# Optimization experiments

Hardware: AMD Instinct MI355X
Metric: run time of the kernel (lower is better)

Reference implementation:

```python
import jax, jax.numpy as jnp
import numpy as np

N = 50000      # nodes
E = 800000     # edges (before self loops)
F_IN = 128     # dataset.num_features
HID = 32       # hidden_channels (per GAT head)
HEADS = 4
C = 40         # dataset.num_classes
NEG_SLOPE = 0.2


def setup_inputs() -> dict:
    key = jax.random.key(0)
    ks = jax.random.split(key, 18)
    g = lambda k, shape, fan: jax.random.normal(k, shape, dtype=jnp.float32) / np.sqrt(fan)
    inp = {
        "x": jax.random.normal(ks[0], (N, F_IN), dtype=jnp.float32),
        "edge_index": jax.random.randint(ks[1], (2, E), 0, N, dtype=jnp.int64),
        # GAT layer 1: F_IN -> HEADS*HID
        "gat_W1": g(ks[2], (F_IN, HEADS * HID), F_IN),
        "gat_att_src1": g(ks[3], (HEADS, HID), HID),
        "gat_att_dst1": g(ks[4], (HEADS, HID), HID),
        "gat_b1": jnp.zeros((HEADS * HID,), jnp.float32),
        # GAT layer 2: HEADS*HID -> C, heads=1
        "gat_W2": g(ks[5], (HEADS * HID, C), HEADS * HID),
        "gat_att_src2": g(ks[6], (1, C), C),
        "gat_att_dst2": g(ks[7], (1, C), C),
        "gat_b2": jnp.zeros((C,), jnp.float32),
        # GCN layers
        "gcn_W1": g(ks[8], (F_IN, HID), F_IN),
        "gcn_b1": jnp.zeros((HID,), jnp.float32),
        "gcn_W2": g(ks[9], (HID, C), HID),
        "gcn_b2": jnp.zeros((C,), jnp.float32),
        # final linear: 2C -> C
        "lin_W": g(ks[10], (2 * C, C), 2 * C),
        "lin_b": jnp.zeros((C,), jnp.float32),
        "weight_c": jnp.float32(0.5),
        "weight_t": jnp.float32(0.5),
    }
    return inp


def _add_self_loops(src, dst, n):
    loop = jnp.arange(n, dtype=src.dtype)
    return jnp.concatenate([src, loop]), jnp.concatenate([dst, loop])


def _gat_conv(x, src, dst, n, W, att_src, att_dst, b, heads, out_dim):
    # h: [n, heads, out_dim]
    h = (x @ W).reshape(n, heads, out_dim)
    a_s = jnp.einsum('nhd,hd->nh', h, att_src)   # source-side attention logit
    a_d = jnp.einsum('nhd,hd->nh', h, att_dst)   # target-side attention logit
    e = jax.nn.leaky_relu(a_s[src] + a_d[dst], NEG_SLOPE)  # [E', heads]
    # softmax over incoming edges of each target node (self loops guarantee >=1 edge)
    m = jax.ops.segment_max(e, dst, num_segments=n)
    ex = jnp.exp(e - m[dst])
    s = jax.ops.segment_sum(ex, dst, num_segments=n)
    alpha = ex / s[dst]                          # [E', heads]
    out = jax.ops.segment_sum(h[src] * alpha[..., None], dst, num_segments=n)
    return out.reshape(n, heads * out_dim) + b


def _gcn_conv(x, src, dst, n, W, b):
    h = x @ W
    deg = jax.ops.segment_sum(jnp.ones(src.shape, h.dtype), dst, num_segments=n)
    norm = jax.lax.rsqrt(deg)                    # deg >= 1 (self loops)
    coef = (norm[src] * norm[dst])[:, None]
    return jax.ops.segment_sum(h[src] * coef, dst, num_segments=n) + b


def reference(x, edge_index, gat_W1, gat_att_src1, gat_att_dst1, gat_b1,
              gat_W2, gat_att_src2, gat_att_dst2, gat_b2,
              gcn_W1, gcn_b1, gcn_W2, gcn_b2, lin_W, lin_b,
              weight_c, weight_t):
    n = x.shape[0]
    src, dst = _add_self_loops(edge_index[0], edge_index[1], n)
    # GAT branch (dropout is identity at inference)
    x_gat = _gat_conv(x, src, dst, n, gat_W1, gat_att_src1, gat_att_dst1,
                      gat_b1, HEADS, HID)
    x_gat = jax.nn.elu(x_gat)
    x_gat = _gat_conv(x_gat, src, dst, n, gat_W2, gat_att_src2, gat_att_dst2,
                      gat_b2, 1, C)
    # GCN branch
    x_gcn = jax.nn.relu(_gcn_conv(x, src, dst, n, gcn_W1, gcn_b1))
    x_gcn = _gcn_conv(x_gcn, src, dst, n, gcn_W2, gcn_b2)
    # weighted feature concat + linear head
    cat = jnp.concatenate([x_gcn * weight_c, x_gat * weight_t], axis=1)  # [n, 2C]
    return cat @ lin_W + lin_b
```

## Files before the change

kernel.cpp:

```cpp
#include <hip/hip_runtime.h>
#include <math.h>

#define F_IN   128
#define HIDC   32
#define NHEAD  4
#define CDIM   40
#define NEG_SLOPE 0.2f
#define BCAP   4096
#define OVCAP  16384
#define SCHUNK 4096

typedef __attribute__((ext_vector_type(8))) short bf16x8;
typedef __attribute__((ext_vector_type(4))) float f32x4;

__device__ __forceinline__ float leakyf(float x) { return x > 0.f ? x : NEG_SLOPE * x; }

__device__ __forceinline__ float wred_sum(float v) {
#pragma unroll
    for (int o = 32; o > 0; o >>= 1) v += __shfl_xor(v, o, 64);
    return v;
}
__device__ __forceinline__ float sel4(float4 v, int h) {
    return (h == 0) ? v.x : (h == 1) ? v.y : (h == 2) ? v.z : v.w;
}
__device__ __forceinline__ unsigned pack2_bf16(float a, float b) {
    unsigned ua = __float_as_uint(a);
    unsigned ub = __float_as_uint(b);
    ua = (ua + 0x7FFFu + ((ua >> 16) & 1u)) >> 16;
    ub = (ub + 0x7FFFu + ((ub >> 16) & 1u)) >> 16;
    return ua | (ub << 16);
}
__device__ __forceinline__ float2 unpack2_bf16(unsigned p) {
    return make_float2(__uint_as_float(p << 16), __uint_as_float(p & 0xFFFF0000u));
}
__device__ __forceinline__ float bf2f(unsigned short u) {
    return __uint_as_float(((unsigned)u) << 16);
}

__global__ void wb_prep_kernel(const float* __restrict__ Wg, const float* __restrict__ Wc,
                               uint4* __restrict__ wbf)
{
    int b = blockIdx.x;
    int lane = threadIdx.x;
    int nt = b >> 2, ks = b & 3;
    int c = nt * 16 + (lane & 15);
    int k0 = ks * 32 + (lane >> 4) * 8;
    unsigned u[4];
#pragma unroll
    for (int jj = 0; jj < 4; ++jj) {
        int k = k0 + 2 * jj;
        float a0 = (c < 128) ? Wg[(size_t)k * 128 + c] : Wc[(size_t)k * 32 + (c - 128)];
        float a1 = (c < 128) ? Wg[(size_t)(k + 1) * 128 + c] : Wc[(size_t)(k + 1) * 32 + (c - 128)];
        u[jj] = pack2_bf16(a0, a1);
    }
    wbf[(size_t)b * 64 + lane] = make_uint4(u[0], u[1], u[2], u[3]);
}

__global__ __launch_bounds__(256) void gemm1_mfma_kernel(
    const float* __restrict__ X, const uint4* __restrict__ wbf,
    const float* __restrict__ aw_s, const float* __restrict__ aw_d,
    unsigned* __restrict__ h1g,
    float* __restrict__ as1, float* __restrict__ ad1, int n)
{
    __shared__ float Ct[64][164];
    __shared__ float sw[128], dw[128];
    const int tid = threadIdx.x;
    const int w = tid >> 6, lane = tid & 63;
    const int m = lane & 15, q = lane >> 4;
    const int node0 = blockIdx.x * 64;
    if (tid < 128) { sw[tid] = aw_s[tid]; dw[tid] = aw_d[tid]; }

    f32x4 acc[10];
#pragma unroll
    for (int t = 0; t < 10; ++t) acc[t] = (f32x4){0.f, 0.f, 0.f, 0.f};

    const int row = node0 + w * 16 + m;
    const bool rv = row < n;
#pragma unroll
    for (int ks = 0; ks < 4; ++ks) {
        uint4 pa = make_uint4(0u, 0u, 0u, 0u);
        if (rv) {
            const float* xr = X + (size_t)row * 128 + ks * 32 + q * 8;
            float4 a0 = *(const float4*)xr;
            float4 a1 = *(const float4*)(xr + 4);
            pa = make_uint4(pack2_bf16(a0.x, a0.y), pack2_bf16(a0.z, a0.w),
                            pack2_bf16(a1.x, a1.y), pack2_bf16(a1.z, a1.w));
        }
        bf16x8 af = *(bf16x8*)&pa;
#pragma unroll
        for (int nt = 0; nt < 10; ++nt) {
            uint4 pb = wbf[(size_t)(nt * 4 + ks) * 64 + lane];
            bf16x8 bfv = *(bf16x8*)&pb;
            acc[nt] = __builtin_amdgcn_mfma_f32_16x16x32_bf16(af, bfv, acc[nt], 0, 0, 0);
        }
    }
#pragma unroll
    for (int nt = 0; nt < 10; ++nt)
#pragma unroll
        for (int r = 0; r < 4; ++r)
            Ct[w * 16 + q * 4 + r][nt * 16 + m] = acc[nt][r];
    __syncthreads();

    for (int i = tid; i < 64 * 80; i += 256) {
        int nd = i / 80, u = i - nd * 80;
        int gn = node0 + nd;
        if (gn < n)
            h1g[(size_t)gn * 80 + u] = pack2_bf16(Ct[nd][2 * u], Ct[nd][2 * u + 1]);
    }
    {
        int nd = tid >> 2, h = tid & 3;
        int gn = node0 + nd;
        if (gn < n) {
            float s = 0.f, d = 0.f;
#pragma unroll
            for (int k = 0; k < HIDC; ++k) {
                float v = Ct[nd][h * HIDC + k];
                s = fmaf(v, sw[h * HIDC + k], s);
                d = fmaf(v, dw[h * HIDC + k], d);
            }
            as1[(size_t)gn * 4 + h] = s;
            ad1[(size_t)gn * 4 + h] = d;
        }
    }
}

__global__ __launch_bounds__(256) void bucket_scatter_kernel(
    const int* __restrict__ src, const int* __restrict__ dst,
    unsigned* __restrict__ bcnt, unsigned* __restrict__ bpair,
    unsigned* __restrict__ ovf_cnt, uint2* __restrict__ ovf, int e, int nbuck)
{
    __shared__ unsigned hist[512];
    __shared__ unsigned base[512];
    const int t = threadIdx.x;
    const int lo = blockIdx.x * SCHUNK;
    const int hi = min(lo + SCHUNK, e);
    for (int i = t; i < nbuck; i += 256) hist[i] = 0;
    __syncthreads();
    for (int i = lo + t; i < hi; i += 256)
        atomicAdd(&hist[((unsigned)dst[i]) >> 7], 1u);
    __syncthreads();
    for (int i = t; i < nbuck; i += 256) {
        unsigned c = hist[i];
        base[i] = c ? atomicAdd(&bcnt[i], c) : 0u;
        hist[i] = 0;
    }
    __syncthreads();
    for (int i = lo + t; i < hi; i += 256) {
        unsigned s = (unsigned)src[i], d = (unsigned)dst[i];
        unsigned b = d >> 7;
        unsigned pos = base[b] + atomicAdd(&hist[b], 1u);
        if (pos < BCAP) bpair[(size_t)b * BCAP + pos] = s | ((d & 127u) << 16);
        else {
            unsigned o = atomicAdd(ovf_cnt, 1u);
            if (o < OVCAP) ovf[o] = make_uint2(s, d);
        }
    }
}

__global__ __launch_bounds__(256) void bucket_count_kernel(
    const unsigned* __restrict__ bcnt, const unsigned* __restrict__ bpair,
    const unsigned* __restrict__ ovf_cnt, const uint2* __restrict__ ovf,
    unsigned* __restrict__ counts, int n)
{
    __shared__ unsigned lc[128];
    const int b = blockIdx.x, base = b << 7;
    if (threadIdx.x < 128) lc[threadIdx.x] = 0;
    __syncthreads();
    unsigned bc = bcnt[b];
    int cnt = (int)(bc < BCAP ? bc : BCAP);
    for (int k = threadIdx.x; k < cnt; k += 256)
        atomicAdd(&lc[bpair[(size_t)b * BCAP + k] >> 16], 1u);
    unsigned oc_u = *ovf_cnt;
    int oc = (int)(oc_u < OVCAP ? oc_u : OVCAP);
    for (int k = threadIdx.x; k < oc; k += 256) {
        uint2 pp = ovf[k];
        if ((int)(pp.y >> 7) == b) atomicAdd(&lc[pp.y & 127u], 1u);
    }
    __syncthreads();
    int i = base + threadIdx.x;
    if (threadIdx.x < 128 && i < n) counts[i] = lc[threadIdx.x];
}

__global__ __launch_bounds__(256) void scan_reduce_kernel(const unsigned* __restrict__ counts,
                                                          unsigned* __restrict__ partials, int n)
{
    __shared__ unsigned sm[256];
    int t = threadIdx.x;
    int i = blockIdx.x * 256 + t;
    unsigned v = (i < n) ? counts[i] : 0u;
    sm[t] = v;
    __syncthreads();
#pragma unroll
    for (int off = 128; off > 0; off >>= 1) {
        if (t < off) sm[t] += sm[t + off];
        __syncthreads();
    }
    if (t == 0) partials[blockIdx.x] = sm[0];
}

__global__ __launch_bounds__(256) void scan_partials_kernel(unsigned* __restrict__ partials,
                                                            unsigned* __restrict__ rs, int nb, int n)
{
    __shared__ unsigned sm[256];
    int t = threadIdx.x;
    unsigned v = (t < nb) ? partials[t] : 0u;
    sm[t] = v;
    __syncthreads();
#pragma unroll
    for (int off = 1; off < 256; off <<= 1) {
        unsigned u = (t >= off) ? sm[t - off] : 0u;
        __syncthreads();
        sm[t] += u;
        __syncthreads();
    }
    if (t < nb) partials[t] = sm[t] - v;
    if (t == 255) rs[n] = sm[255];
}

__global__ __launch_bounds__(256) void scan_write_kernel(const unsigned* __restrict__ counts,
                                                         const unsigned* __restrict__ partials,
                                                         unsigned* __restrict__ rs,
                                                         float* __restrict__ nrm, int n)
{
    __shared__ unsigned sm[256];
    int t = threadIdx.x;
    int i = blockIdx.x * 256 + t;
    unsigned c = (i < n) ? counts[i] : 0u;
    sm[t] = c;
    __syncthreads();
#pragma unroll
    for (int off = 1; off < 256; off <<= 1) {
        unsigned u = (t >= off) ? sm[t - off] : 0u;
        __syncthreads();
        sm[t] += u;
        __syncthreads();
    }
    if (i < n) {
        rs[i] = partials[blockIdx.x] + sm[t] - c;
        nrm[i] = rsqrtf((float)(c + 1u));
    }
}

__global__ __launch_bounds__(256) void bucket_place_kernel(
    const unsigned* __restrict__ bcnt, const unsigned* __restrict__ bpair,
    const unsigned* __restrict__ rs, unsigned* __restrict__ csr_src,
    unsigned* __restrict__ cursor, int n)
{
    __shared__ unsigned lc[128];
    __shared__ unsigned rbase[128];
    const int b = blockIdx.x, base = b << 7;
    if (threadIdx.x < 128) {
        lc[threadIdx.x] = 0;
        int i = base + threadIdx.x;
        rbase[threadIdx.x] = (i < n) ? rs[i] : 0u;
    }
    __syncthreads();
    unsigned bc = bcnt[b];
    int cnt = (int)(bc < BCAP ? bc : BCAP);
    for (int k = threadIdx.x; k < cnt; k += 256) {
        unsigned v = bpair[(size_t)b * BCAP + k];
        unsigned ld = v >> 16;
        unsigned r = atomicAdd(&lc[ld], 1u);
        csr_src[rbase[ld] + r] = v & 0xFFFFu;
    }
    __syncthreads();
    int i = base + threadIdx.x;
    if (threadIdx.x < 128 && i < n) cursor[i] = rbase[threadIdx.x] + lc[threadIdx.x];
}

__global__ void overflow_fill_kernel(const unsigned* __restrict__ ovf_cnt,
                                     const uint2* __restrict__ ovf,
                                     unsigned* __restrict__ cursor,
                                     unsigned* __restrict__ csr_src)
{
    unsigned oc_u = *ovf_cnt;
    int oc = (int)(oc_u < OVCAP ? oc_u : OVCAP);
    for (int k = threadIdx.x; k < oc; k += 256) {
        uint2 pp = ovf[k];
        unsigned pos = atomicAdd(&cursor[pp.y], 1u);
        csr_src[pos] = pp.x;
    }
}

#define CAP1 96
__global__ __launch_bounds__(256) void agg1_fused_kernel(
    const unsigned* __restrict__ h1g,
    const float* __restrict__ as1, const float* __restrict__ ad1,
    const float* __restrict__ nrm,
    const unsigned* __restrict__ rs, const unsigned* __restrict__ csr_src,
    const float* __restrict__ gat_b1, const float* __restrict__ gcn_b1,
    unsigned* __restrict__ xgb, unsigned* __restrict__ gaccb, int n)
{
    __shared__ uint2 scA[4][CAP1];
    __shared__ float w4[4][CAP1][4];
    const int wid = threadIdx.x >> 6;
    const int lane = threadIdx.x & 63;
    const int i = blockIdx.x * 4 + wid;
    if (i >= n) return;
    const unsigned beg = rs[i];
    const int deg = (int)(rs[i + 1] - beg);
    const float4* as1v = (const float4*)as1;
    float4 av = as1v[i];
    float4 dv = ((const float4*)ad1)[i];
    const float ni = nrm[i];
    float4 ese = make_float4(__expf(leakyf(av.x + dv.x)), __expf(leakyf(av.y + dv.y)),
                             __expf(leakyf(av.z + dv.z)), __expf(leakyf(av.w + dv.w)));
    float s0 = 0.f, s1 = 0.f, s2 = 0.f, s3 = 0.f;
    for (int k = lane; k < deg; k += 64) {
        unsigned s = csr_src[beg + k];
        float4 a = as1v[s];
        float w0 = __expf(leakyf(a.x + dv.x)), w1 = __expf(leakyf(a.y + dv.y));
        float w2 = __expf(leakyf(a.z + dv.z)), w3 = __expf(leakyf(a.w + dv.w));
        if (k < CAP1) {
            scA[wid][k] = make_uint2(s, __float_as_uint(nrm[s]));
            w4[wid][k][0] = w0; w4[wid][k][1] = w1;
            w4[wid][k][2] = w2; w4[wid][k][3] = w3;
        }
        s0 += w0; s1 += w1; s2 += w2; s3 += w3;
    }
    if (lane == 0) { s0 += ese.x; s1 += ese.y; s2 += ese.z; s3 += ese.w; }
    s0 = wred_sum(s0); s1 = wred_sum(s1); s2 = wred_sum(s2); s3 = wred_sum(s3);
    __threadfence_block();
    const int h = lane >> 4;
    const float advh = sel4(dv, h);
    const float ssh  = sel4(make_float4(s0, s1, s2, s3), h);
    const float wself = sel4(ese, h);
    const bool gact = lane < 32;
    const unsigned short* h1s = (const unsigned short*)h1g;
    float2 hv = unpack2_bf16(h1g[(size_t)i * 80 + lane]);
    float2 acc = make_float2(hv.x * wself, hv.y * wself);
    float gacc = gact ? bf2f(h1s[(size_t)i * 160 + 128 + lane]) * ni * ni : 0.f;
    const int dcB = deg < CAP1 ? deg : CAP1;
    int j = 0;
    for (; j + 4 <= dcB; j += 4) {
        uint2 sc[4]; float ww[4];
#pragma unroll
        for (int t = 0; t < 4; ++t) {
            sc[t] = scA[wid][j + t];
            ww[t] = w4[wid][j + t][h];
        }
        unsigned pv[4];
#pragma unroll
        for (int t = 0; t < 4; ++t) pv[t] = h1g[(size_t)sc[t].x * 80 + lane];
        float gv[4];
        if (gact) {
#pragma unroll
            for (int t = 0; t < 4; ++t) gv[t] = bf2f(h1s[(size_t)sc[t].x * 160 + 128 + lane]);
        }
#pragma unroll
        for (int t = 0; t < 4; ++t) {
            float2 v = unpack2_bf16(pv[t]);
            acc.x = fmaf(v.x, ww[t], acc.x);
            acc.y = fmaf(v.y, ww[t], acc.y);
            if (gact) gacc = fmaf(gv[t], __uint_as_float(sc[t].y) * ni, gacc);
        }
    }
    for (; j < dcB; ++j) {
        uint2 sc = scA[wid][j];
        float w = w4[wid][j][h];
        float2 v = unpack2_bf16(h1g[(size_t)sc.x * 80 + lane]);
        acc.x = fmaf(v.x, w, acc.x);
        acc.y = fmaf(v.y, w, acc.y);
        if (gact) gacc = fmaf(bf2f(h1s[(size_t)sc.x * 160 + 128 + lane]),
                              __uint_as_float(sc.y) * ni, gacc);
    }
    for (; j < deg; ++j) {
        unsigned s = csr_src[beg + j];
        float4 a = as1v[s];
        float w = __expf(leakyf(sel4(a, h) + advh));
        float c = nrm[s];
        float2 v = unpack2_bf16(h1g[(size_t)s * 80 + lane]);
        acc.x = fmaf(v.x, w, acc.x);
        acc.y = fmaf(v.y, w, acc.y);
        if (gact) gacc = fmaf(bf2f(h1s[(size_t)s * 160 + 128 + lane]), c * ni, gacc);
    }
    float inv = 1.f / ssh;
    int c0 = 2 * lane;
    float o0 = acc.x * inv + gat_b1[c0];
    float o1 = acc.y * inv + gat_b1[c0 + 1];
    o0 = o0 > 0.f ? o0 : __expf(o0) - 1.f;
    o1 = o1 > 0.f ? o1 : __expf(o1) - 1.f;
    xgb[(size_t)i * 64 + lane] = pack2_bf16(o0, o1);
    float go = gact ? fmaxf(gacc + gcn_b1[lane], 0.f) : 0.f;
    float gp = __shfl_xor(go, 1, 64);
    if (gact && (lane & 1) == 0)
        gaccb[(size_t)i * 16 + (lane >> 1)] = pack2_bf16(go, gp);
}

__global__ __launch_bounds__(320) void gemm2_fused_kernel(
    const unsigned* __restrict__ xgb, const unsigned* __restrict__ gaccb,
    const float* __restrict__ Wgat, const float* __restrict__ Wgcn,
    const float* __restrict__ aw_s, const float* __restrict__ aw_d,
    unsigned* __restrict__ hg_b, float* __restrict__ as2, float* __restrict__ ad2, int n)
{
    constexpr int BN = 128, NT = 320, CG = 10;
    __shared__ float smem[32 * 132 + 32 * 40];
    float* Xs = smem;
    float* Ws = smem + 32 * 132;
    const int tid = threadIdx.x;
    const int cg = tid % CG, ng = tid / CG;
    const int node0 = blockIdx.x * BN;

    {
        float acc[4][4] = {};
        for (int idx = tid; idx < BN * 4; idx += NT) {
            int nd = idx >> 2, kq = idx & 3;
            int gnode = node0 + nd;
            uint4 v = (gnode < n) ? *(const uint4*)&gaccb[(size_t)gnode * 16 + kq * 4]
                                  : make_uint4(0u, 0u, 0u, 0u);
            float2 a = unpack2_bf16(v.x), b = unpack2_bf16(v.y);
            float2 c = unpack2_bf16(v.z), d = unpack2_bf16(v.w);
            Xs[(kq * 8 + 0) * 132 + nd] = a.x; Xs[(kq * 8 + 1) * 132 + nd] = a.y;
            Xs[(kq * 8 + 2) * 132 + nd] = b.x; Xs[(kq * 8 + 3) * 132 + nd] = b.y;
            Xs[(kq * 8 + 4) * 132 + nd] = c.x; Xs[(kq * 8 + 5) * 132 + nd] = c.y;
            Xs[(kq * 8 + 6) * 132 + nd] = d.x; Xs[(kq * 8 + 7) * 132 + nd] = d.y;
        }
        for (int idx = tid; idx < 32 * CG; idx += NT) {
            int kk = idx / CG, cq = idx % CG;
            *(float4*)&Ws[kk * 40 + cq * 4] = *(const float4*)&Wgcn[(size_t)kk * 40 + cq * 4];
        }
        __syncthreads();
#pragma unroll
        for (int k = 0; k < 32; ++k) {
            float4 xv = *(const float4*)&Xs[k * 132 + ng * 4];
            float4 wv = *(const float4*)&Ws[k * 40 + cg * 4];
            float xa[4] = {xv.x, xv.y, xv.z, xv.w};
            float wa[4] = {wv.x, wv.y, wv.z, wv.w};
#pragma unroll
            for (int j = 0; j < 4; ++j)
#pragma unroll
                for (int c = 0; c < 4; ++c)
                    acc[j][c] = fmaf(xa[j], wa[c], acc[j][c]);
        }
        __syncthreads();
#pragma unroll
        for (int j = 0; j < 4; ++j) {
            int gnode = node0 + ng * 4 + j;
            if (gnode < n) {
                uint2 pb = make_uint2(pack2_bf16(acc[j][0], acc[j][1]),
                                      pack2_bf16(acc[j][2], acc[j][3]));
                *(uint2*)&hg_b[(size_t)gnode * 40 + 20 + cg * 2] = pb;
            }
        }
    }

    float acc[4][4] = {};
    for (int kb = 0; kb < 128; kb += 32) {
        for (int idx = tid; idx < BN * 4; idx += NT) {
            int nd = idx >> 2, kq = idx & 3;
            int gnode = node0 + nd;
            uint4 v = (gnode < n) ? *(const uint4*)&xgb[(size_t)gnode * 64 + kb / 2 + kq * 4]
                                  : make_uint4(0u, 0u, 0u, 0u);
            float2 a = unpack2_bf16(v.x), b = unpack2_bf16(v.y);
            float2 c = unpack2_bf16(v.z), d = unpack2_bf16(v.w);
            Xs[(kq * 8 + 0) * 132 + nd] = a.x; Xs[(kq * 8 + 1) * 132 + nd] = a.y;
            Xs[(kq * 8 + 2) * 132 + nd] = b.x; Xs[(kq * 8 + 3) * 132 + nd] = b.y;
            Xs[(kq * 8 + 4) * 132 + nd] = c.x; Xs[(kq * 8 + 5) * 132 + nd] = c.y;
            Xs[(kq * 8 + 6) * 132 + nd] = d.x; Xs[(kq * 8 + 7) * 132 + nd] = d.y;
        }
        for (int idx = tid; idx < 32 * CG; idx += NT) {
            int kk = idx / CG, cq = idx % CG;
            *(float4*)&Ws[kk * 40 + cq * 4] = *(const float4*)&Wgat[(size_t)(kb + kk) * 40 + cq * 4];
        }
        __syncthreads();
#pragma unroll
        for (int k = 0; k < 32; ++k) {
            float4 xv = *(const float4*)&Xs[k * 132 + ng * 4];
            float4 wv = *(const float4*)&Ws[k * 40 + cg * 4];
            float xa[4] = {xv.x, xv.y, xv.z, xv.w};
            float wa[4] = {wv.x, wv.y, wv.z, wv.w};
#pragma unroll
            for (int j = 0; j < 4; ++j)
#pragma unroll
                for (int c = 0; c < 4; ++c)
                    acc[j][c] = fmaf(xa[j], wa[c], acc[j][c]);
        }
        __syncthreads();
    }

    float* Ct  = smem;
    float* sww = smem + 128 * 41;
    float* dww = sww + 40;
#pragma unroll
    for (int j = 0; j < 4; ++j) {
        int gnode = node0 + ng * 4 + j;
        if (gnode < n) {
            uint2 pb = make_uint2(pack2_bf16(acc[j][0], acc[j][1]),
                                  pack2_bf16(acc[j][2], acc[j][3]));
            *(uint2*)&hg_b[(size_t)gnode * 40 + cg * 2] = pb;
        }
#pragma unroll
        for (int c = 0; c < 4; ++c)
            Ct[(ng * 4 + j) * 41 + cg * 4 + c] = acc[j][c];
    }
    if (tid < 40) { sww[tid] = aw_s[tid]; dww[tid] = aw_d[tid]; }
    __syncthreads();
    if (tid < 128) {
        int gnode = node0 + tid;
        if (gnode < n) {
            float s = 0.f, d = 0.f;
#pragma unroll
            for (int c = 0; c < 40; ++c) {
                float v = Ct[tid * 41 + c];
                s = fmaf(v, sww[c], s);
                d = fmaf(v, dww[c], d);
            }
            as2[gnode] = s;
            ad2[gnode] = d;
        }
    }
}

#define CAP2 128
__global__ __launch_bounds__(256) void agg2_fused_kernel(
    const unsigned* __restrict__ hg_b, const float* __restrict__ as2,
    const float* __restrict__ ad2, const float* __restrict__ nrm,
    const unsigned* __restrict__ rs, const unsigned* __restrict__ csr_src,
    const float* __restrict__ gat_b2, const float* __restrict__ gcn_b2,
    const float* __restrict__ wc_p, const float* __restrict__ wt_p,
    unsigned* __restrict__ catb, int n)
{
    __shared__ unsigned sidx[4][CAP2];
    __shared__ float    wgt[4][CAP2];
    __shared__ float    cf [4][CAP2];
    const int wid = threadIdx.x >> 6;
    const int lane = threadIdx.x & 63;
    const int i = blockIdx.x * 4 + wid;
    if (i >= n) return;
    const unsigned beg = rs[i];
    const int deg = (int)(rs[i + 1] - beg);
    const float adv = ad2[i];
    const float eself = __expf(leakyf(as2[i] + adv));
    const float ni = nrm[i];
    float ssum = (lane == 0) ? eself : 0.f;
    for (int k = lane; k < deg; k += 64) {
        unsigned s = csr_src[beg + k];
        float w = __expf(leakyf(as2[s] + adv));
        if (k < CAP2) { sidx[wid][k] = s; wgt[wid][k] = w; cf[wid][k] = nrm[s]; }
        ssum += w;
    }
    ssum = wred_sum(ssum);
    __threadfence_block();
    const bool act   = lane < 40;
    const bool isgat = lane < 20;
    const float selfw = isgat ? eself : ni * ni;
    float2 acc = make_float2(0.f, 0.f);
    if (act) {
        float2 v = unpack2_bf16(hg_b[(size_t)i * 40 + lane]);
        acc.x = v.x * selfw; acc.y = v.y * selfw;
    }
    const int dcB = deg < CAP2 ? deg : CAP2;
    int j = 0;
    for (; j + 4 <= dcB; j += 4) {
        unsigned ss[4]; float ww[4];
#pragma unroll
        for (int t = 0; t < 4; ++t) {
            ss[t] = sidx[wid][j + t];
            ww[t] = isgat ? wgt[wid][j + t] : cf[wid][j + t] * ni;
        }
        if (act) {
#pragma unroll
            for (int t = 0; t < 4; ++t) {
                float2 v = unpack2_bf16(hg_b[(size_t)ss[t] * 40 + lane]);
                acc.x = fmaf(v.x, ww[t], acc.x);
                acc.y = fmaf(v.y, ww[t], acc.y);
            }
        }
    }
    for (; j < dcB; ++j) {
        unsigned s = sidx[wid][j];
        float w = isgat ? wgt[wid][j] : cf[wid][j] * ni;
        if (act) {
            float2 v = unpack2_bf16(hg_b[(size_t)s * 40 + lane]);
            acc.x = fmaf(v.x, w, acc.x); acc.y = fmaf(v.y, w, acc.y);
        }
    }
    for (; j < deg; ++j) {
        unsigned s = csr_src[beg + j];
        float w = isgat ? __expf(leakyf(as2[s] + adv)) : nrm[s] * ni;
        if (act) {
            float2 v = unpack2_bf16(hg_b[(size_t)s * 40 + lane]);
            acc.x = fmaf(v.x, w, acc.x); acc.y = fmaf(v.y, w, acc.y);
        }
    }
    if (act) {
        if (isgat) {
            float inv = 1.f / ssum, wt = *wt_p;
            int c0 = 2 * lane;
            catb[(size_t)i * 40 + 20 + lane] =
                pack2_bf16((acc.x * inv + gat_b2[c0]) * wt,
                           (acc.y * inv + gat_b2[c0 + 1]) * wt);
        } else {
            float wc = *wc_p;
            int c0 = 2 * (lane - 20);
            catb[(size_t)i * 40 + (lane - 20)] =
                pack2_bf16((acc.x + gcn_b2[c0]) * wc,
                           (acc.y + gcn_b2[c0 + 1]) * wc);
        }
    }
}

__global__ __launch_bounds__(320) void gemm_head_kernel(
    const unsigned* __restrict__ catb, const float* __restrict__ W,
    const float* __restrict__ bias, float* __restrict__ out, int n)
{
    constexpr int BN = 128, NT = 320, CG = 10, BK = 40;
    __shared__ float Xs[BK][BN + 4];
    __shared__ float Ws[BK][40];
    const int tid = threadIdx.x;
    const int cg = tid % CG, ng = tid / CG;
    const int node0 = blockIdx.x * BN;
    float acc[4][4] = {};

    for (int kb = 0; kb < 80; kb += BK) {
        for (int idx = tid; idx < BN * 5; idx += NT) {
            int nd = idx / 5, kq = idx - nd * 5;
            int gnode = node0 + nd;
            uint4 v = (gnode < n) ? *(const uint4*)&catb[(size_t)gnode * 40 + kb / 2 + kq * 4]
                                  : make_uint4(0u, 0u, 0u, 0u);
            float2 a = unpack2_bf16(v.x), b = unpack2_bf16(v.y);
            float2 c = unpack2_bf16(v.z), d = unpack2_bf16(v.w);
            Xs[kq * 8 + 0][nd] = a.x; Xs[kq * 8 + 1][nd] = a.y;
            Xs[kq * 8 + 2][nd] = b.x; Xs[kq * 8 + 3][nd] = b.y;
            Xs[kq * 8 + 4][nd] = c.x; Xs[kq * 8 + 5][nd] = c.y;
            Xs[kq * 8 + 6][nd] = d.x; Xs[kq * 8 + 7][nd] = d.y;
        }
        for (int idx = tid; idx < BK * CG; idx += NT) {
            int kk = idx / CG, cq = idx % CG;
            *(float4*)&Ws[kk][cq * 4] = *(const float4*)&W[(size_t)(kb + kk) * 40 + cq * 4];
        }
        __syncthreads();
#pragma unroll
        for (int k = 0; k < BK; ++k) {
            float4 xv = *(const float4*)&Xs[k][ng * 4];
            float4 wv = *(const float4*)&Ws[k][cg * 4];
            float xa[4] = {xv.x, xv.y, xv.z, xv.w};
            float wa[4] = {wv.x, wv.y, wv.z, wv.w};
#pragma unroll
            for (int j = 0; j < 4; ++j)
#pragma unroll
                for (int c = 0; c < 4; ++c)
                    acc[j][c] = fmaf(xa[j], wa[c], acc[j][c]);
        }
        __syncthreads();
    }

    float4 bv = *(const float4*)&bias[cg * 4];
#pragma unroll
    for (int j = 0; j < 4; ++j) {
        int gnode = node0 + ng * 4 + j;
        if (gnode < n) {
            float4 o = make_float4(acc[j][0] + bv.x, acc[j][1] + bv.y,
                                   acc[j][2] + bv.z, acc[j][3] + bv.w);
            *(float4*)&out[(size_t)gnode * 40 + cg * 4] = o;
        }
    }
}

extern "C" void kernel_launch(void* const* d_in, const int* in_sizes, int n_in,
                              void* d_out, int out_size, void* d_ws, size_t ws_size,
                              hipStream_t stream)
{
    const float* x        = (const float*)d_in[0];
    const int*   eidx     = (const int*)d_in[1];
    const float* gat_W1   = (const float*)d_in[2];
    const float* att_s1   = (const float*)d_in[3];
    const float* att_d1   = (const float*)d_in[4];
    const float* gat_b1   = (const float*)d_in[5];
    const float* gat_W2   = (const float*)d_in[6];
    const float* att_s2   = (const float*)d_in[7];
    const float* att_d2   = (const float*)d_in[8];
    const float* gat_b2   = (const float*)d_in[9];
    const float* gcn_W1   = (const float*)d_in[10];
    const float* gcn_b1   = (const float*)d_in[11];
    const float* gcn_W2   = (const float*)d_in[12];
    const float* gcn_b2   = (const float*)d_in[13];
    const float* lin_W    = (const float*)d_in[14];
    const float* lin_b    = (const float*)d_in[15];
    const float* wc_p     = (const float*)d_in[16];
    const float* wt_p     = (const float*)d_in[17];

    const int n = in_sizes[0] / F_IN;
    const int e = in_sizes[1] / 2;
    const int* src = eidx;
    const int* dst = eidx + e;
    const int NBUCK = (n + 127) >> 7;

    char* p = (char*)d_ws;
    auto alloc = [&](size_t bytes) -> void* {
        void* r = (void*)p;
        p += (bytes + 255) & ~(size_t)255;
        return r;
    };
    unsigned* counts  = (unsigned*)alloc((size_t)n * 4);
    unsigned* rs      = (unsigned*)alloc((size_t)(n + 1) * 4);
    unsigned* cursor  = (unsigned*)alloc((size_t)n * 4);
    unsigned* partials= (unsigned*)alloc(256 * 4);
    unsigned* bcnt    = (unsigned*)alloc((size_t)(NBUCK + 1) * 4);
    unsigned* csr_src = (unsigned*)alloc((size_t)e * 4);
    uint4*    wbf     = (uint4*)alloc(40 * 64 * 16);
    float* nrm     = (float*)alloc((size_t)n * 4);
    float* as1     = (float*)alloc((size_t)n * 4 * 4);
    float* ad1     = (float*)alloc((size_t)n * 4 * 4);
    float* as2     = (float*)alloc((size_t)n * 4);
    float* ad2     = (float*)alloc((size_t)n * 4);
    unsigned* regA = (unsigned*)alloc((size_t)n * 80 * 4);
    unsigned* hg_b = (unsigned*)alloc((size_t)n * 40 * 4);
    unsigned* xgb  = (unsigned*)alloc((size_t)n * 64 * 4);
    unsigned* gaccb= (unsigned*)alloc((size_t)n * 16 * 4);
    unsigned* bpair = regA;
    uint2*    ovf   = (uint2*)(bpair + (size_t)NBUCK * BCAP);
    unsigned* h1g   = regA;
    unsigned* catb  = regA;
    unsigned* ovf_cnt = bcnt + NBUCK;

    const int NB = (n + 255) / 256;
    const int WB = (n + 3) / 4;
    const int SB = (e + SCHUNK - 1) / SCHUNK;

    hipMemsetAsync(bcnt, 0, (size_t)(NBUCK + 1) * 4, stream);
    bucket_scatter_kernel<<<SB, 256, 0, stream>>>(src, dst, bcnt, bpair, ovf_cnt, ovf, e, NBUCK);
    bucket_count_kernel<<<NBUCK, 256, 0, stream>>>(bcnt, bpair, ovf_cnt, ovf, counts, n);
    scan_reduce_kernel<<<NB, 256, 0, stream>>>(counts, partials, n);
    scan_partials_kernel<<<1, 256, 0, stream>>>(partials, rs, NB, n);
    scan_write_kernel<<<NB, 256, 0, stream>>>(counts, partials, rs, nrm, n);
    bucket_place_kernel<<<NBUCK, 256, 0, stream>>>(bcnt, bpair, rs, csr_src, cursor, n);
    overflow_fill_kernel<<<1, 256, 0, stream>>>(ovf_cnt, ovf, cursor, csr_src);

    wb_prep_kernel<<<40, 64, 0, stream>>>(gat_W1, gcn_W1, wbf);
    gemm1_mfma_kernel<<<(n + 63) / 64, 256, 0, stream>>>(x, wbf, att_s1, att_d1,
                                                         h1g, as1, ad1, n);

    agg1_fused_kernel<<<WB, 256, 0, stream>>>(h1g, as1, ad1, nrm, rs, csr_src,
                                              gat_b1, gcn_b1, xgb, gaccb, n);

    gemm2_fused_kernel<<<(n + 127) / 128, 320, 0, stream>>>(xgb, gaccb, gat_W2, gcn_W2,
                                                            att_s2, att_d2, hg_b, as2, ad2, n);

    agg2_fused_kernel<<<WB, 256, 0, stream>>>(hg_b, as2, ad2, nrm, rs, csr_src,
                                              gat_b2, gcn_b2, wc_p, wt_p, catb, n);

    gemm_head_kernel<<<(n + 127) / 128, 320, 0, stream>>>(catb, lin_W, lin_b, (float*)d_out, n);
}
```

Baseline: 313.4 us.

## Fuse CSR count, scan and placement into bucket-level prefix and build kernels

Replaces the five-kernel CSR construction (per-node count, three-stage node scan, placement) with two kernels. The first is a single-block scan over per-bucket edge totals. The second is a per-bucket kernel that stages the bucket's pairs in shared memory, counts per node, scans locally, writes row starts and norms, and places sources. This removes three kernel launches, the global counts and partials arrays, and a second global read of the bucket pairs. In exchange each build block uses 16KB of shared memory, and the single-block prefix assumes at most 512 buckets.

```diff
diff --git a/kernel.cpp b/kernel.cpp
--- a/kernel.cpp
+++ b/kernel.cpp
@@ -157,115 +157,85 @@
     }
 }
 
-__global__ __launch_bounds__(256) void bucket_count_kernel(
+__global__ __launch_bounds__(512) void bucket_prefix_kernel(
+    const unsigned* __restrict__ bcnt, unsigned* __restrict__ bprefix,
+    unsigned* __restrict__ rs, int nbuck, int n, unsigned e)
+{
+    __shared__ unsigned sm[512];
+    int t = threadIdx.x;
+    unsigned v = (t < nbuck) ? bcnt[t] : 0u;
+    sm[t] = v;
+    __syncthreads();
+#pragma unroll
+    for (int off = 1; off < 512; off <<= 1) {
+        unsigned u = (t >= off) ? sm[t - off] : 0u;
+        __syncthreads();
+        sm[t] += u;
+        __syncthreads();
+    }
+    if (t < nbuck) bprefix[t] = sm[t] - v;
+    if (t == 0) rs[n] = e;
+}
+
+__global__ __launch_bounds__(256) void bucket_build_kernel(
     const unsigned* __restrict__ bcnt, const unsigned* __restrict__ bpair,
+    const unsigned* __restrict__ bprefix,
     const unsigned* __restrict__ ovf_cnt, const uint2* __restrict__ ovf,
-    unsigned* __restrict__ counts, int n)
-{
-    __shared__ unsigned lc[128];
+    unsigned* __restrict__ rs, float* __restrict__ nrm,
+    unsigned* __restrict__ csr_src, unsigned* __restrict__ cursor, int n)
+{
+    __shared__ unsigned sp[BCAP];
+    __shared__ unsigned lc[128], ex[128], plc[128];
     const int b = blockIdx.x, base = b << 7;
-    if (threadIdx.x < 128) lc[threadIdx.x] = 0;
+    const int tid = threadIdx.x;
+    if (tid < 128) { lc[tid] = 0; plc[tid] = 0; }
     __syncthreads();
     unsigned bc = bcnt[b];
     int cnt = (int)(bc < BCAP ? bc : BCAP);
-    for (int k = threadIdx.x; k < cnt; k += 256)
-        atomicAdd(&lc[bpair[(size_t)b * BCAP + k] >> 16], 1u);
+    for (int k = tid; k < cnt; k += 256) {
+        unsigned v = bpair[(size_t)b * BCAP + k];
+        sp[k] = v;
+        atomicAdd(&lc[v >> 16], 1u);
+    }
     unsigned oc_u = *ovf_cnt;
     int oc = (int)(oc_u < OVCAP ? oc_u : OVCAP);
-    for (int k = threadIdx.x; k < oc; k += 256) {
+    for (int k = tid; k < oc; k += 256) {
         uint2 pp = ovf[k];
         if ((int)(pp.y >> 7) == b) atomicAdd(&lc[pp.y & 127u], 1u);
     }
     __syncthreads();
-    int i = base + threadIdx.x;
-    if (threadIdx.x < 128 && i < n) counts[i] = lc[threadIdx.x];
-}
-
-__global__ __launch_bounds__(256) void scan_reduce_kernel(const unsigned* __restrict__ counts,
-                                                          unsigned* __restrict__ partials, int n)
-{
-    __shared__ unsigned sm[256];
-    int t = threadIdx.x;
-    int i = blockIdx.x * 256 + t;
-    unsigned v = (i < n) ? counts[i] : 0u;
-    sm[t] = v;
-    __syncthreads();
-#pragma unroll
-    for (int off = 128; off > 0; off >>= 1) {
-        if (t < off) sm[t] += sm[t + off];
-        __syncthreads();
-    }
-    if (t == 0) partials[blockIdx.x] = sm[0];
-}
-
-__global__ __launch_bounds__(256) void scan_partials_kernel(unsigned* __restrict__ partials,
-                                                            unsigned* __restrict__ rs, int nb, int n)
-{
-    __shared__ unsigned sm[256];
-    int t = threadIdx.x;
-    unsigned v = (t < nb) ? partials[t] : 0u;
-    sm[t] = v;
-    __syncthreads();
-#pragma unroll
-    for (int off = 1; off < 256; off <<= 1) {
-        unsigned u = (t >= off) ? sm[t - off] : 0u;
-        __syncthreads();
-        sm[t] += u;
-        __syncthreads();
-    }
-    if (t < nb) partials[t] = sm[t] - v;
-    if (t == 255) rs[n] = sm[255];
-}
-
-__global__ __launch_bounds__(256) void scan_write_kernel(const unsigned* __restrict__ counts,
-                                                         const unsigned* __restrict__ partials,
-                                                         unsigned* __restrict__ rs,
-                                                         float* __restrict__ nrm, int n)
-{
-    __shared__ unsigned sm[256];
-    int t = threadIdx.x;
-    int i = blockIdx.x * 256 + t;
-    unsigned c = (i < n) ? counts[i] : 0u;
-    sm[t] = c;
-    __syncthreads();
-#pragma unroll
-    for (int off = 1; off < 256; off <<= 1) {
-        unsigned u = (t >= off) ? sm[t - off] : 0u;
-        __syncthreads();
-        sm[t] += u;
-        __syncthreads();
-    }
-    if (i < n) {
-        rs[i] = partials[blockIdx.x] + sm[t] - c;
-        nrm[i] = rsqrtf((float)(c + 1u));
-    }
-}
-
-__global__ __launch_bounds__(256) void bucket_place_kernel(
-    const unsigned* __restrict__ bcnt, const unsigned* __restrict__ bpair,
-    const unsigned* __restrict__ rs, unsigned* __restrict__ csr_src,
-    unsigned* __restrict__ cursor, int n)
-{
-    __shared__ unsigned lc[128];
-    __shared__ unsigned rbase[128];
-    const int b = blockIdx.x, base = b << 7;
-    if (threadIdx.x < 128) {
-        lc[threadIdx.x] = 0;
-        int i = base + threadIdx.x;
-        rbase[threadIdx.x] = (i < n) ? rs[i] : 0u;
-    }
-    __syncthreads();
-    unsigned bc = bcnt[b];
-    int cnt = (int)(bc < BCAP ? bc : BCAP);
-    for (int k = threadIdx.x; k < cnt; k += 256) {
-        unsigned v = bpair[(size_t)b * BCAP + k];
+    unsigned myc = (tid < 128) ? lc[tid] : 0u;
+    if (tid < 128) ex[tid] = myc;
+    __syncthreads();
+#pragma unroll
+    for (int off = 1; off < 128; off <<= 1) {
+        unsigned u = (tid < 128 && tid >= off) ? ex[tid - off] : 0u;
+        __syncthreads();
+        if (tid < 128) ex[tid] += u;
+        __syncthreads();
+    }
+    if (tid < 128) ex[tid] -= myc;
+    __syncthreads();
+    const unsigned bp = bprefix[b];
+    if (tid < 128) {
+        int i = base + tid;
+        if (i < n) {
+            rs[i]  = bp + ex[tid];
+            nrm[i] = rsqrtf((float)(lc[tid] + 1u));
+        }
+    }
+    __syncthreads();
+    for (int k = tid; k < cnt; k += 256) {
+        unsigned v = sp[k];
         unsigned ld = v >> 16;
-        unsigned r = atomicAdd(&lc[ld], 1u);
-        csr_src[rbase[ld] + r] = v & 0xFFFFu;
-    }
-    __syncthreads();
-    int i = base + threadIdx.x;
-    if (threadIdx.x < 128 && i < n) cursor[i] = rbase[threadIdx.x] + lc[threadIdx.x];
+        unsigned r = atomicAdd(&plc[ld], 1u);
+        csr_src[bp + ex[ld] + r] = v & 0xFFFFu;
+    }
+    __syncthreads();
+    if (tid < 128) {
+        int i = base + tid;
+        if (i < n) cursor[i] = bp + ex[tid] + plc[tid];
+    }
 }
 
 __global__ void overflow_fill_kernel(const unsigned* __restrict__ ovf_cnt,
@@ -692,11 +662,10 @@
         p += (bytes + 255) & ~(size_t)255;
         return r;
     };
-    unsigned* counts  = (unsigned*)alloc((size_t)n * 4);
     unsigned* rs      = (unsigned*)alloc((size_t)(n + 1) * 4);
     unsigned* cursor  = (unsigned*)alloc((size_t)n * 4);
-    unsigned* partials= (unsigned*)alloc(256 * 4);
     unsigned* bcnt    = (unsigned*)alloc((size_t)(NBUCK + 1) * 4);
+    unsigned* bprefix = (unsigned*)alloc((size_t)NBUCK * 4);
     unsigned* csr_src = (unsigned*)alloc((size_t)e * 4);
     uint4*    wbf     = (uint4*)alloc(40 * 64 * 16);
     float* nrm     = (float*)alloc((size_t)n * 4);
@@ -714,17 +683,14 @@
     unsigned* catb  = regA;
     unsigned* ovf_cnt = bcnt + NBUCK;
 
-    const int NB = (n + 255) / 256;
     const int WB = (n + 3) / 4;
     const int SB = (e + SCHUNK - 1) / SCHUNK;
 
     hipMemsetAsync(bcnt, 0, (size_t)(NBUCK + 1) * 4, stream);
     bucket_scatter_kernel<<<SB, 256, 0, stream>>>(src, dst, bcnt, bpair, ovf_cnt, ovf, e, NBUCK);
-    bucket_count_kernel<<<NBUCK, 256, 0, stream>>>(bcnt, bpair, ovf_cnt, ovf, counts, n);
-    scan_reduce_kernel<<<NB, 256, 0, stream>>>(counts, partials, n);
-    scan_partials_kernel<<<1, 256, 0, stream>>>(partials, rs, NB, n);
-    scan_write_kernel<<<NB, 256, 0, stream>>>(counts, partials, rs, nrm, n);
-    bucket_place_kernel<<<NBUCK, 256, 0, stream>>>(bcnt, bpair, rs, csr_src, cursor, n);
+    bucket_prefix_kernel<<<1, 512, 0, stream>>>(bcnt, bprefix, rs, NBUCK, n, (unsigned)e);
+    bucket_build_kernel<<<NBUCK, 256, 0, stream>>>(bcnt, bpair, bprefix, ovf_cnt, ovf,
+                                                   rs, nrm, csr_src, cursor, n);
     overflow_fill_kernel<<<1, 256, 0, stream>>>(ovf_cnt, ovf, cursor, csr_src);
 
     wb_prep_kernel<<<40, 64, 0, stream>>>(gat_W1, gcn_W1, wbf);
```

Result: faster. 305.5 us (-2.5%).
